# Optimization experiments

Measured on AMD Instinct MI355X. Metric: run time of the kernel, lower is better.

Reference implementation:

```python
import jax, jax.numpy as jnp
import numpy as np

B, T, D, O = 16, 1024, 1024, 10  # broadcast in original requires T == D

def setup_inputs() -> dict:
    key = jax.random.key(0)
    k1, k2, k3 = jax.random.split(key, 3)
    logits = jax.random.normal(k1, (B, T, D), dtype=jnp.float32)
    decision = jax.random.uniform(k2, (B, T, O), dtype=jnp.float32)  # unused by forward math
    W = jax.random.normal(k3, (O, D), dtype=jnp.float32) * 0.02  # attention.weight
    b = jnp.zeros((O,), dtype=jnp.float32)                       # attention.bias
    return {"logits": logits, "decision": decision, "W": W, "b": b}

def reference(logits, decision, W, b):
    outputdim = W.shape[0]
    # w_x = softmax(Linear(logits)/outputdim, dim=1)  -> softmax over time T
    scores = (jnp.einsum('btd,od->bto', logits, W) + b) / outputdim  # (B,T,O)
    w_x = jax.nn.softmax(scores, axis=1)
    # Original materializes h[b,i,o,t] = logits[b,t,i] * w_x[b,i,o] (needs T==D),
    # then flattens (o,t) and sums over dim 1 (i). Equivalent contraction:
    # out[b,o,t] = sum_i logits[b,t,i] * w_x[b,i,o]
    out = jnp.einsum('bti,bio->bot', logits, w_x)  # (B,O,T)
    return out.reshape(logits.shape[0], -1)        # (B, O*T)
```

## Files before the change

kernel.cpp:

```cpp
#include <hip/hip_runtime.h>

#define BB 16
#define TT 1024
#define DD 1024
#define OO 10

template <bool BIAS>
__global__ __launch_bounds__(256) void gemm10_kernel(
    const float* __restrict__ X,
    const float* __restrict__ Wt,
    const float* __restrict__ bias,
    float* __restrict__ Y,
    float scale, int perBatchW)
{
    __shared__ float4 sW4[OO * 256];
    __shared__ float4 sX[2][32 * 33];
    __shared__ float  part[4][32][OO];

    const int b   = blockIdx.y;
    const int t0  = blockIdx.x * 32;
    const int tid = threadIdx.x;

    {
        const float4* src = (const float4*)(Wt + (size_t)(perBatchW ? b : 0) * (OO * DD));
#pragma unroll
        for (int c = 0; c < 10; ++c)
            sW4[c * 256 + tid] = src[c * 256 + tid];
    }

    const int srow = tid >> 5;
    const int scol = tid & 31;
    const float4* Xb = (const float4*)(X + ((size_t)b * TT + t0) * DD);

    {
        float4 st[4];
#pragma unroll
        for (int k = 0; k < 4; ++k)
            st[k] = Xb[(size_t)(srow + 8 * k) * 256 + scol];
#pragma unroll
        for (int k = 0; k < 4; ++k)
            sX[0][(srow + 8 * k) * 33 + scol] = st[k];
    }
    __syncthreads();

    const int w    = tid >> 6;
    const int lane = tid & 63;
    const int l    = lane & 7;
    const int g    = lane >> 3;
    const int xoff = w * 8 + l;

    float acc[4][OO];
#pragma unroll
    for (int j = 0; j < 4; ++j)
#pragma unroll
        for (int o = 0; o < OO; ++o) acc[j][o] = 0.f;

#pragma unroll 1
    for (int c = 0; c < 8; ++c) {
        float4 st[4];
        if (c < 7) {
#pragma unroll
            for (int k = 0; k < 4; ++k)
                st[k] = Xb[(size_t)(srow + 8 * k) * 256 + (c + 1) * 32 + scol];
        }

        const float4* xb = sX[c & 1];
        float4 xf[4];
#pragma unroll
        for (int j = 0; j < 4; ++j)
            xf[j] = xb[(g + 8 * j) * 33 + xoff];
#pragma unroll
        for (int o = 0; o < OO; ++o) {
            const float4 wv = sW4[o * 256 + c * 32 + xoff];
#pragma unroll
            for (int j = 0; j < 4; ++j)
                acc[j][o] += xf[j].x * wv.x + xf[j].y * wv.y +
                             xf[j].z * wv.z + xf[j].w * wv.w;
        }

        if (c < 7) {
#pragma unroll
            for (int k = 0; k < 4; ++k)
                sX[(c + 1) & 1][(srow + 8 * k) * 33 + scol] = st[k];
        }
        __syncthreads();
    }

#pragma unroll
    for (int j = 0; j < 4; ++j) {
#pragma unroll
        for (int o = 0; o < OO; ++o) {
            float v = acc[j][o];
            v += __shfl_down(v, 4, 8);
            v += __shfl_down(v, 2, 8);
            v += __shfl_down(v, 1, 8);
            if (l == 0) part[w][j * 8 + g][o] = v;
        }
    }
    __syncthreads();

    for (int idx = tid; idx < 32 * OO; idx += 256) {
        const int row = idx / OO;
        const int o   = idx % OO;
        float v = part[0][row][o] + part[1][row][o] +
                  part[2][row][o] + part[3][row][o];
        if (BIAS) v = (v + bias[o]) * scale;
        Y[((size_t)b * OO + o) * TT + (t0 + row)] = v;
    }
}

__global__ __launch_bounds__(256) void softmax_kernel(float* __restrict__ s)
{
    float* col = s + (size_t)blockIdx.x * TT;
    const int tid  = threadIdx.x;
    const int wave = tid >> 6;
    const int lane = tid & 63;

    float4 v = *(const float4*)(col + tid * 4);

    __shared__ float sm[4];
    __shared__ float ss[4];

    float m = fmaxf(fmaxf(v.x, v.y), fmaxf(v.z, v.w));
#pragma unroll
    for (int off = 32; off > 0; off >>= 1) m = fmaxf(m, __shfl_down(m, off, 64));
    if (lane == 0) sm[wave] = m;
    __syncthreads();
    m = fmaxf(fmaxf(sm[0], sm[1]), fmaxf(sm[2], sm[3]));

    float e0 = __expf(v.x - m), e1 = __expf(v.y - m);
    float e2 = __expf(v.z - m), e3 = __expf(v.w - m);
    float sum = e0 + e1 + e2 + e3;
#pragma unroll
    for (int off = 32; off > 0; off >>= 1) sum += __shfl_down(sum, off, 64);
    if (lane == 0) ss[wave] = sum;
    __syncthreads();
    const float inv = 1.0f / (ss[0] + ss[1] + ss[2] + ss[3]);

    *(float4*)(col + tid * 4) = make_float4(e0 * inv, e1 * inv, e2 * inv, e3 * inv);
}

extern "C" void kernel_launch(void* const* d_in, const int* in_sizes, int n_in,
                              void* d_out, int out_size, void* d_ws, size_t ws_size,
                              hipStream_t stream)
{
    const float* logits = (const float*)d_in[0];
    const float* W    = (const float*)d_in[2];
    const float* bias = (const float*)d_in[3];
    float* out    = (float*)d_out;
    float* scores = (float*)d_ws;

    dim3 grid(TT / 32, BB);
    gemm10_kernel<true><<<grid, 256, 0, stream>>>(logits, W, bias, scores,
                                                  1.0f / OO, 0);
    softmax_kernel<<<BB * OO, 256, 0, stream>>>(scores);
    gemm10_kernel<false><<<grid, 256, 0, stream>>>(logits, scores, nullptr, out,
                                                   1.0f, 1);
}
```

Before: 144.4 us.

## Fuse softmax into second GEMM and stream X directly from global into registers

Removes the separate softmax kernel: each block of the second GEMM now loads its batch's 10x1024 scores, computes max/sum reductions and writes normalized weights into shared memory. The X tile is no longer staged through shared memory with double buffering; each thread loads its float4 slices straight from global into register banks, prefetching the next chunk while computing. This saves a launch and a round trip of the scores, but every block of the second GEMM redundantly recomputes the softmax for its batch, and register pressure goes up.

```diff
diff --git a/kernel.cpp b/kernel.cpp
--- a/kernel.cpp
+++ b/kernel.cpp
@@ -5,49 +5,120 @@
 #define DD 1024
 #define OO 10
 
-template <bool BIAS>
+
+#define STEP_FMA(bank, stepexpr)                                          \
+    {                                                                     \
+        float4 c[4];                                                      \
+        _Pragma("unroll") for (int j = 0; j < 4; ++j) c[j] = bank[j];     \
+        if (it == 0) {                                                    \
+            _Pragma("unroll") for (int j = 0; j < 4; ++j)                 \
+                bank[j] = *(const float4*)(xp[j] + ((stepexpr) + 4) * 32);\
+        }                                                                 \
+        const float* wp = sWl + (stepexpr) * 32;                          \
+        _Pragma("unroll") for (int o = 0; o < OO; ++o) {                  \
+            const float4 wv = *(const float4*)(wp + o * DD);              \
+            _Pragma("unroll") for (int j = 0; j < 4; ++j)                 \
+                acc[j][o] += c[j].x * wv.x + c[j].y * wv.y +              \
+                             c[j].z * wv.z + c[j].w * wv.w;               \
+        }                                                                 \
+    }
+
+template <bool FIRST>
 __global__ __launch_bounds__(256) void gemm10_kernel(
     const float* __restrict__ X,
-    const float* __restrict__ Wt,
+    const float* __restrict__ Wsrc,
     const float* __restrict__ bias,
-    float* __restrict__ Y,
-    float scale, int perBatchW)
+    float* __restrict__ Y)
 {
     __shared__ float4 sW4[OO * 256];
-    __shared__ float4 sX[2][32 * 33];
     __shared__ float  part[4][32][OO];
+    __shared__ float  red[4][OO];
 
-    const int b   = blockIdx.y;
-    const int t0  = blockIdx.x * 32;
-    const int tid = threadIdx.x;
-
-    {
-        const float4* src = (const float4*)(Wt + (size_t)(perBatchW ? b : 0) * (OO * DD));
-#pragma unroll
-        for (int c = 0; c < 10; ++c)
-            sW4[c * 256 + tid] = src[c * 256 + tid];
-    }
-
-    const int srow = tid >> 5;
-    const int scol = tid & 31;
-    const float4* Xb = (const float4*)(X + ((size_t)b * TT + t0) * DD);
-
-    {
-        float4 st[4];
-#pragma unroll
-        for (int k = 0; k < 4; ++k)
-            st[k] = Xb[(size_t)(srow + 8 * k) * 256 + scol];
-#pragma unroll
-        for (int k = 0; k < 4; ++k)
-            sX[0][(srow + 8 * k) * 33 + scol] = st[k];
-    }
-    __syncthreads();
-
+    const int b    = blockIdx.y;
+    const int t0   = blockIdx.x * 32;
+    const int tid  = threadIdx.x;
     const int w    = tid >> 6;
     const int lane = tid & 63;
     const int l    = lane & 7;
     const int g    = lane >> 3;
-    const int xoff = w * 8 + l;
+    const int dofs = w * 256 + l * 4;
+
+    const float* xp[4];
+#pragma unroll
+    for (int j = 0; j < 4; ++j)
+        xp[j] = X + ((size_t)b * TT + t0 + g + 8 * j) * DD + dofs;
+
+    float4 x0[4], x1[4], x2[4], x3[4];
+#pragma unroll
+    for (int j = 0; j < 4; ++j) {
+        x0[j] = *(const float4*)(xp[j]);
+        x1[j] = *(const float4*)(xp[j] + 32);
+        x2[j] = *(const float4*)(xp[j] + 64);
+        x3[j] = *(const float4*)(xp[j] + 96);
+    }
+
+    if (FIRST) {
+        const float4* src = (const float4*)Wsrc;
+#pragma unroll
+        for (int c = 0; c < 10; ++c)
+            sW4[c * 256 + tid] = src[c * 256 + tid];
+        __syncthreads();
+    } else {
+        const float* sb = Wsrc + (size_t)b * OO * TT;
+        float4 sv[OO];
+        float  mo[OO];
+#pragma unroll
+        for (int o = 0; o < OO; ++o) {
+            const float* p = sb + (size_t)o * TT + tid * 4;
+            float4 v = make_float4(p[0], p[1], p[2], p[3]);
+            sv[o] = v;
+            mo[o] = fmaxf(fmaxf(v.x, v.y), fmaxf(v.z, v.w));
+        }
+#pragma unroll
+        for (int o = 0; o < OO; ++o) {
+            float m = mo[o];
+#pragma unroll
+            for (int off = 32; off > 0; off >>= 1)
+                m = fmaxf(m, __shfl_down(m, off, 64));
+            if (lane == 0) red[w][o] = m;
+        }
+        __syncthreads();
+        float M[OO];
+#pragma unroll
+        for (int o = 0; o < OO; ++o)
+            M[o] = fmaxf(fmaxf(red[0][o], red[1][o]),
+                         fmaxf(red[2][o], red[3][o]));
+        __syncthreads();
+        float so[OO];
+#pragma unroll
+        for (int o = 0; o < OO; ++o) {
+            float4 v = sv[o];
+            v.x = __expf(v.x - M[o]); v.y = __expf(v.y - M[o]);
+            v.z = __expf(v.z - M[o]); v.w = __expf(v.w - M[o]);
+            sv[o] = v;
+            so[o] = v.x + v.y + v.z + v.w;
+        }
+#pragma unroll
+        for (int o = 0; o < OO; ++o) {
+            float s = so[o];
+#pragma unroll
+            for (int off = 32; off > 0; off >>= 1)
+                s += __shfl_down(s, off, 64);
+            if (lane == 0) red[w][o] = s;
+        }
+        __syncthreads();
+#pragma unroll
+        for (int o = 0; o < OO; ++o) {
+            const float inv = 1.0f / (red[0][o] + red[1][o] +
+                                      red[2][o] + red[3][o]);
+            float4 v = sv[o];
+            sW4[o * 256 + tid] =
+                make_float4(v.x * inv, v.y * inv, v.z * inv, v.w * inv);
+        }
+        __syncthreads();
+    }
+
+    const float* sWl = (const float*)sW4 + dofs;
 
     float acc[4][OO];
 #pragma unroll
@@ -56,38 +127,15 @@
         for (int o = 0; o < OO; ++o) acc[j][o] = 0.f;
 
 #pragma unroll 1
-    for (int c = 0; c < 8; ++c) {
-        float4 st[4];
-        if (c < 7) {
-#pragma unroll
-            for (int k = 0; k < 4; ++k)
-                st[k] = Xb[(size_t)(srow + 8 * k) * 256 + (c + 1) * 32 + scol];
-        }
-
-        const float4* xb = sX[c & 1];
-        float4 xf[4];
-#pragma unroll
-        for (int j = 0; j < 4; ++j)
-            xf[j] = xb[(g + 8 * j) * 33 + xoff];
-#pragma unroll
-        for (int o = 0; o < OO; ++o) {
-            const float4 wv = sW4[o * 256 + c * 32 + xoff];
-#pragma unroll
-            for (int j = 0; j < 4; ++j)
-                acc[j][o] += xf[j].x * wv.x + xf[j].y * wv.y +
-                             xf[j].z * wv.z + xf[j].w * wv.w;
-        }
-
-        if (c < 7) {
-#pragma unroll
-            for (int k = 0; k < 4; ++k)
-                sX[(c + 1) & 1][(srow + 8 * k) * 33 + scol] = st[k];
-        }
-        __syncthreads();
+    for (int it = 0; it < 8; it += 4) {
+        STEP_FMA(x0, it + 0)
+        STEP_FMA(x1, it + 1)
+        STEP_FMA(x2, it + 2)
+        STEP_FMA(x3, it + 3)
     }
 
 #pragma unroll
-    for (int j = 0; j < 4; ++j) {
+    for (int j = 0; j < 4; ++j)
 #pragma unroll
         for (int o = 0; o < OO; ++o) {
             float v = acc[j][o];
@@ -96,7 +144,6 @@
             v += __shfl_down(v, 1, 8);
             if (l == 0) part[w][j * 8 + g][o] = v;
         }
-    }
     __syncthreads();
 
     for (int idx = tid; idx < 32 * OO; idx += 256) {
@@ -104,40 +151,9 @@
         const int o   = idx % OO;
         float v = part[0][row][o] + part[1][row][o] +
                   part[2][row][o] + part[3][row][o];
-        if (BIAS) v = (v + bias[o]) * scale;
+        if (FIRST) v = (v + bias[o]) * (1.0f / OO);
         Y[((size_t)b * OO + o) * TT + (t0 + row)] = v;
     }
-}
-
-__global__ __launch_bounds__(256) void softmax_kernel(float* __restrict__ s)
-{
-    float* col = s + (size_t)blockIdx.x * TT;
-    const int tid  = threadIdx.x;
-    const int wave = tid >> 6;
-    const int lane = tid & 63;
-
-    float4 v = *(const float4*)(col + tid * 4);
-
-    __shared__ float sm[4];
-    __shared__ float ss[4];
-
-    float m = fmaxf(fmaxf(v.x, v.y), fmaxf(v.z, v.w));
-#pragma unroll
-    for (int off = 32; off > 0; off >>= 1) m = fmaxf(m, __shfl_down(m, off, 64));
-    if (lane == 0) sm[wave] = m;
-    __syncthreads();
-    m = fmaxf(fmaxf(sm[0], sm[1]), fmaxf(sm[2], sm[3]));
-
-    float e0 = __expf(v.x - m), e1 = __expf(v.y - m);
-    float e2 = __expf(v.z - m), e3 = __expf(v.w - m);
-    float sum = e0 + e1 + e2 + e3;
-#pragma unroll
-    for (int off = 32; off > 0; off >>= 1) sum += __shfl_down(sum, off, 64);
-    if (lane == 0) ss[wave] = sum;
-    __syncthreads();
-    const float inv = 1.0f / (ss[0] + ss[1] + ss[2] + ss[3]);
-
-    *(float4*)(col + tid * 4) = make_float4(e0 * inv, e1 * inv, e2 * inv, e3 * inv);
 }
 
 extern "C" void kernel_launch(void* const* d_in, const int* in_sizes, int n_in,
@@ -151,9 +167,6 @@
     float* scores = (float*)d_ws;
 
     dim3 grid(TT / 32, BB);
-    gemm10_kernel<true><<<grid, 256, 0, stream>>>(logits, W, bias, scores,
-                                                  1.0f / OO, 0);
-    softmax_kernel<<<BB * OO, 256, 0, stream>>>(scores);
-    gemm10_kernel<false><<<grid, 256, 0, stream>>>(logits, scores, nullptr, out,
-                                                   1.0f, 1);
+    gemm10_kernel<true><<<grid, 256, 0, stream>>>(logits, W, bias, scores);
+    gemm10_kernel<false><<<grid, 256, 0, stream>>>(logits, scores, nullptr, out);
 }
```

Result: faster. 140.0 us (-3.1%).
